# Kernel tuning notes

Measured on AMD Instinct MI355X. Metric: run time of the kernel, lower is better.

## Reference

```python
import jax, jax.numpy as jnp
import numpy as np

B, L, H, DI, N, R, K = 1, 1024, 2048, 4096, 16, 128, 4


def setup_inputs() -> dict:
    key = jax.random.key(0)
    ks = jax.random.split(key, 12)
    s = 0.02
    x = jax.random.normal(ks[0], (B, L, H), jnp.float32)
    W_in_states = jax.random.normal(ks[1], (DI, H), jnp.float32) * s
    W_in_gates = jax.random.normal(ks[2], (DI, H), jnp.float32) * s
    conv_w = jax.random.normal(ks[3], (DI, K), jnp.float32) * 0.2
    conv_b = jax.random.normal(ks[4], (DI,), jnp.float32) * 0.02
    W_dt = jax.random.normal(ks[5], (R, DI), jnp.float32) * s
    W_b = jax.random.normal(ks[6], (N, DI), jnp.float32) * s
    W_c = jax.random.normal(ks[7], (N, DI), jnp.float32) * s
    W_dtproj = jax.random.normal(ks[8], (DI, R), jnp.float32) * 0.1
    # dt bias so softplus(dt) is in a realistic small range
    b_dtproj = jax.random.uniform(ks[9], (DI,), jnp.float32, minval=-5.0, maxval=-3.0)
    A_log = jnp.log(jnp.broadcast_to(jnp.arange(1, N + 1, dtype=jnp.float32), (DI, N)))
    D = jnp.ones((DI,), jnp.float32)
    W_out = jax.random.normal(ks[10], (H, DI), jnp.float32) * s
    return {"x": x, "W_in_states": W_in_states, "W_in_gates": W_in_gates,
            "conv_w": conv_w, "conv_b": conv_b, "W_dt": W_dt, "W_b": W_b,
            "W_c": W_c, "W_dtproj": W_dtproj, "b_dtproj": b_dtproj,
            "A_log": A_log, "D": D, "W_out": W_out}


def _silu(v):
    return v * jax.nn.sigmoid(v)


def reference(x, W_in_states, W_in_gates, conv_w, conv_b, W_dt, W_b, W_c,
              W_dtproj, b_dtproj, A_log, D, W_out):
    b, l, _ = x.shape
    # input projections -> [B, DI, L]
    hs = jnp.einsum('blh,dh->bdl', x, W_in_states)
    gate = jnp.einsum('blh,dh->bdl', x, W_in_gates)
    # causal depthwise conv1d (kernel K, left pad K-1, truncate to L)
    k = conv_w.shape[-1]
    xpad = jnp.pad(hs, ((0, 0), (0, 0), (k - 1, 0)))
    conv = sum(conv_w[None, :, j, None] * xpad[:, :, j:j + l] for j in range(k))
    conv = conv + conv_b[None, :, None]
    hs = _silu(conv)                       # [B, DI, L]
    hst = hs.transpose(0, 2, 1)            # [B, L, DI]
    # data-dependent SSM params
    time_step = jnp.einsum('bld,rd->blr', hst, W_dt)           # [B, L, R]
    dt = jax.nn.softplus(time_step @ W_dtproj.T + b_dtproj)    # [B, L, DI]
    Bm = jnp.einsum('bld,nd->bln', hst, W_b)                   # [B, L, N]
    Cm = jnp.einsum('bld,nd->bln', hst, W_c)                   # [B, L, N]
    A = -jnp.exp(A_log)                                        # [DI, N]
    dt_bdl = dt.transpose(0, 2, 1)                             # [B, DI, L]
    dA = jnp.exp(A[None, :, None, :] * dt_bdl[:, :, :, None])  # [B, DI, L, N]
    dBu = dt_bdl[:, :, :, None] * Bm[:, None, :, :] * hs[:, :, :, None]
    # sequential selective scan over L
    dA_l = dA.transpose(2, 0, 1, 3)    # [L, B, DI, N]
    dBu_l = dBu.transpose(2, 0, 1, 3)

    def step(s, inp):
        a, bu = inp
        s = a * s + bu
        return s, s

    init = jnp.zeros((b, hs.shape[1], A_log.shape[1]), hs.dtype)
    _, h = jax.lax.scan(step, init, (dA_l, dBu_l))   # [L, B, DI, N]
    y = jnp.einsum('lbdn,bln->bdl', h, Cm)           # contract state dim
    y = y + hs * D[None, :, None]
    y = y * _silu(gate)
    out = jnp.einsum('bdl,od->blo', y, W_out)        # [B, L, H]
    return out
```

## Files before the change

### kernel.cpp

```cpp
#include <hip/hip_runtime.h>

#define SEQ 1024
#define HID 2048
#define DIN 4096
#define NST 16
#define RNK 128
#define CHN 32
#define CLEN 32

typedef __attribute__((ext_vector_type(4))) float f32x4;
typedef __attribute__((ext_vector_type(4))) __bf16 bf16x4v;
typedef __attribute__((ext_vector_type(8))) __bf16 bf16x8v;
typedef __attribute__((ext_vector_type(8))) unsigned short u16x8;

#define GPTR(p) ((const __attribute__((address_space(1))) void*)(p))
#define LPTR(p) ((__attribute__((address_space(3))) void*)(p))

__device__ __forceinline__ unsigned short f2bf(float v) {
  unsigned u = __builtin_bit_cast(unsigned, v);
  u = (u + 0x7fffu + ((u >> 16) & 1u)) >> 16;
  return (unsigned short)u;
}
__device__ __forceinline__ float softplus_f(float x) {
  return (x > 20.f) ? x : log1pf(__expf(x));
}
__device__ __forceinline__ float silu_f(float x) {
  return x / (1.f + __expf(-x));
}

#define CV_NX  (SEQ*HID)
#define CV_NW  (DIN*HID)
#define CV_NDT (RNK*DIN)
#define CV_NB  (NST*DIN)
#define CV_NPD (32*DIN)
#define CV_NWO (HID*DIN)
#define CV_TOT (CV_NX + 2*CV_NW + CV_NDT + 2*CV_NB + CV_NPD + CV_NDT + CV_NWO)

__global__ __launch_bounds__(256) void cvt_all(
    const float* __restrict__ x, const float* __restrict__ wis,
    const float* __restrict__ wig, const float* __restrict__ wdt,
    const float* __restrict__ wb, const float* __restrict__ wc,
    const float* __restrict__ wdtp, const float* __restrict__ wout,
    unsigned short* __restrict__ x_bf, unsigned short* __restrict__ wis_bf,
    unsigned short* __restrict__ wig_bf, unsigned short* __restrict__ wcat_bf,
    unsigned short* __restrict__ wdtp_bf, unsigned short* __restrict__ wout_bf)
{
  size_t j = ((size_t)blockIdx.x * 256 + threadIdx.x) * 16;
  const float* src = nullptr; unsigned short* dst;
  if (j < CV_NX) { src = x + j; dst = x_bf + j; }
  else if ((j -= CV_NX) < CV_NW) { src = wis + j; dst = wis_bf + j; }
  else if ((j -= CV_NW) < CV_NW) { src = wig + j; dst = wig_bf + j; }
  else if ((j -= CV_NW) < CV_NDT) { src = wdt + j; dst = wcat_bf + j; }
  else if ((j -= CV_NDT) < CV_NB) { src = wb + j; dst = wcat_bf + (size_t)128*DIN + j; }
  else if ((j -= CV_NB) < CV_NB) { src = wc + j; dst = wcat_bf + (size_t)144*DIN + j; }
  else if ((j -= CV_NB) < CV_NPD) { dst = wcat_bf + (size_t)160*DIN + j; }
  else if ((j -= CV_NPD) < CV_NDT) { src = wdtp + j; dst = wdtp_bf + j; }
  else { j -= CV_NDT; src = wout + j; dst = wout_bf + j; }
  u16x8 o0 = {}, o1 = {};
  if (src) {
    f32x4 a = *(const f32x4*)src;
    f32x4 b = *(const f32x4*)(src + 4);
    f32x4 c = *(const f32x4*)(src + 8);
    f32x4 d = *(const f32x4*)(src + 12);
#pragma unroll
    for (int i = 0; i < 4; i++) {
      o0[i] = f2bf(a[i]); o0[4 + i] = f2bf(b[i]);
      o1[i] = f2bf(c[i]); o1[4 + i] = f2bf(d[i]);
    }
  }
  *(u16x8*)dst = o0;
  *(u16x8*)(dst + 8) = o1;
}

template<int EPI>
__global__ __launch_bounds__(256) void gemm128(
    const unsigned short* __restrict__ Ag, const unsigned short* __restrict__ Bg,
    float* __restrict__ Cg, const float* __restrict__ bias,
    int Msz, int Nsz, int Kstride, int Kiter)
{
  __shared__ __align__(16) unsigned short As[2][128 * 64];
  __shared__ __align__(16) unsigned short Bs[2][128 * 64];
  const int kz = blockIdx.z;
  Ag += (size_t)kz * Kiter;
  Bg += (size_t)kz * Kiter;
  Cg += (size_t)kz * Msz * Nsz;
  const int nwg = gridDim.x * gridDim.y;
  const int orig = blockIdx.y * gridDim.x + blockIdx.x;
  const int swz = (orig & 7) * (nwg >> 3) + (orig >> 3);
  const int bx = swz % gridDim.x, by = swz / gridDim.x;
  const int tid = threadIdx.x;
  const int m0 = bx * 128, n0 = by * 128;
  const int lane = tid & 63, w = tid >> 6;
  const int wm = w >> 1, wn = w & 1;
  const int lg = lane >> 4, lr = lane & 15;
  const int srow = w * 32 + (lane >> 3);
  const int sslot = (lane & 7) ^ (lane >> 3);
  const unsigned short* Ag0 = Ag + (size_t)(m0 + srow) * Kstride + sslot * 8;
  const unsigned short* Bg0 = Bg + (size_t)(n0 + srow) * Kstride + sslot * 8;
  const int ldso = w * 2048;

  auto stage = [&](int b, int k0) {
#pragma unroll
    for (int i = 0; i < 4; i++)
      __builtin_amdgcn_global_load_lds(GPTR(Ag0 + (size_t)(i * 8) * Kstride + k0),
                                       LPTR(&As[b][ldso + i * 512]), 16, 0, 0);
#pragma unroll
    for (int i = 0; i < 4; i++)
      __builtin_amdgcn_global_load_lds(GPTR(Bg0 + (size_t)(i * 8) * Kstride + k0),
                                       LPTR(&Bs[b][ldso + i * 512]), 16, 0, 0);
  };

  const int nt = Kiter >> 6;
  stage(0, 0);
  f32x4 acc[4][4] = {};
  int cur = 0;
  const int rsw = lr & 7;
  for (int t = 0; t < nt; ++t) {
    asm volatile("s_waitcnt vmcnt(0)" ::: "memory");
    __builtin_amdgcn_s_barrier();
    asm volatile("" ::: "memory");
    if (t + 1 < nt) stage(cur ^ 1, (t + 1) * 64);
    bf16x8v af0[4], bf0[4], af1[4], bf1[4];
#pragma unroll
    for (int mi = 0; mi < 4; mi++) {
      const int row = (wm * 64 + mi * 16 + lr) * 64;
      af0[mi] = *(const bf16x8v*)&As[cur][row + ((0 * 4 + lg) ^ rsw) * 8];
      af1[mi] = *(const bf16x8v*)&As[cur][row + ((1 * 4 + lg) ^ rsw) * 8];
    }
#pragma unroll
    for (int ni = 0; ni < 4; ni++) {
      const int row = (wn * 64 + ni * 16 + lr) * 64;
      bf0[ni] = *(const bf16x8v*)&Bs[cur][row + ((0 * 4 + lg) ^ rsw) * 8];
      bf1[ni] = *(const bf16x8v*)&Bs[cur][row + ((1 * 4 + lg) ^ rsw) * 8];
    }
#pragma unroll
    for (int mi = 0; mi < 4; mi++)
#pragma unroll
      for (int ni = 0; ni < 4; ni++)
        acc[mi][ni] = __builtin_amdgcn_mfma_f32_16x16x32_bf16(af0[mi], bf0[ni], acc[mi][ni], 0, 0, 0);
#pragma unroll
    for (int mi = 0; mi < 4; mi++)
#pragma unroll
      for (int ni = 0; ni < 4; ni++)
        acc[mi][ni] = __builtin_amdgcn_mfma_f32_16x16x32_bf16(af1[mi], bf1[ni], acc[mi][ni], 0, 0, 0);
    cur ^= 1;
  }
#pragma unroll
  for (int mi = 0; mi < 4; mi++) {
#pragma unroll
    for (int ni = 0; ni < 4; ni++) {
      const int col = n0 + wn * 64 + ni * 16 + lr;
#pragma unroll
      for (int r = 0; r < 4; r++) {
        const int row = m0 + wm * 64 + mi * 16 + lg * 4 + r;
        float v = acc[mi][ni][r];
        if (EPI == 1) v = softplus_f(v + bias[col]);
        Cg[(size_t)row * Nsz + col] = v;
      }
    }
  }
}

template<int EPI>
__global__ __launch_bounds__(256) void gemm_nt(
    const unsigned short* __restrict__ Ag, const unsigned short* __restrict__ Bg,
    float* __restrict__ Cg, const float* __restrict__ bias,
    int Msz, int Nsz, int Kstride, int Kiter)
{
  __shared__ __align__(16) unsigned short As[128][40];
  __shared__ __align__(16) unsigned short Bs[64][40];
  const int kz = blockIdx.z;
  Ag += (size_t)kz * Kiter;
  Bg += (size_t)kz * Kiter;
  Cg += (size_t)kz * Msz * Nsz;
  const int tid = threadIdx.x;
  const int m0 = blockIdx.x * 128, n0 = blockIdx.y * 64;
  const int lane = tid & 63, w = tid >> 6;
  const int wm = w >> 1, wn = w & 1;
  const int lg = lane >> 4, lr = lane & 15;
  const int r4 = tid >> 2, c8 = (tid & 3) * 8;
  f32x4 acc[4][2] = {};
  for (int k0 = 0; k0 < Kiter; k0 += 32) {
    uint4 a0 = *(const uint4*)(Ag + (size_t)(m0 + r4) * Kstride + k0 + c8);
    uint4 a1 = *(const uint4*)(Ag + (size_t)(m0 + 64 + r4) * Kstride + k0 + c8);
    uint4 b0 = *(const uint4*)(Bg + (size_t)(n0 + r4) * Kstride + k0 + c8);
    *(uint4*)&As[r4][c8] = a0;
    *(uint4*)&As[64 + r4][c8] = a1;
    *(uint4*)&Bs[r4][c8] = b0;
    __syncthreads();
    bf16x8v af[4], bfr[2];
#pragma unroll
    for (int mi = 0; mi < 4; mi++) {
      const int row = wm * 64 + mi * 16 + lr;
      bf16x4v lo = *(const bf16x4v*)&As[row][4 * lg];
      bf16x4v hi = *(const bf16x4v*)&As[row][16 + 4 * lg];
      af[mi] = __builtin_shufflevector(lo, hi, 0, 1, 2, 3, 4, 5, 6, 7);
    }
#pragma unroll
    for (int ni = 0; ni < 2; ni++) {
      const int row = wn * 32 + ni * 16 + lr;
      bf16x4v lo = *(const bf16x4v*)&Bs[row][4 * lg];
      bf16x4v hi = *(const bf16x4v*)&Bs[row][16 + 4 * lg];
      bfr[ni] = __builtin_shufflevector(lo, hi, 0, 1, 2, 3, 4, 5, 6, 7);
    }
#pragma unroll
    for (int mi = 0; mi < 4; mi++)
#pragma unroll
      for (int ni = 0; ni < 2; ni++)
        acc[mi][ni] = __builtin_amdgcn_mfma_f32_16x16x32_bf16(af[mi], bfr[ni], acc[mi][ni], 0, 0, 0);
    __syncthreads();
  }
#pragma unroll
  for (int mi = 0; mi < 4; mi++) {
#pragma unroll
    for (int ni = 0; ni < 2; ni++) {
      const int col = n0 + wn * 32 + ni * 16 + lr;
#pragma unroll
      for (int r = 0; r < 4; r++) {
        const int row = m0 + wm * 64 + mi * 16 + lg * 4 + r;
        float v = acc[mi][ni][r];
        if (EPI == 1) v = softplus_f(v + bias[col]);
        Cg[(size_t)row * Nsz + col] = v;
      }
    }
  }
}

__global__ __launch_bounds__(256) void conv_silu(
    const float* __restrict__ pg, const float* __restrict__ cw,
    const float* __restrict__ cb, float* __restrict__ hs,
    unsigned short* __restrict__ hs_bf)
{
  int idx = blockIdx.x * 256 + threadIdx.x;
  int l = idx >> 12, d = idx & (DIN - 1);
  float acc = cb[d];
#pragma unroll
  for (int j = 0; j < 4; j++) {
    int ll = l + j - 3;
    float v = (ll >= 0) ? pg[(size_t)ll * 8192 + d] : 0.f;
    acc = fmaf(cw[d * 4 + j], v, acc);
  }
  float r = silu_f(acc);
  hs[idx] = r;
  hs_bf[idx] = f2bf(r);
}

__global__ __launch_bounds__(256) void reduce_ts(
    const float* __restrict__ c2p, float* __restrict__ c2,
    unsigned short* __restrict__ ts_bf)
{
  int i = blockIdx.x * 256 + threadIdx.x;
  float s = 0.f;
#pragma unroll
  for (int z = 0; z < 8; z++) s += c2p[(size_t)z * SEQ * 192 + i];
  c2[i] = s;
  int l = i / 192, col = i - l * 192;
  if (col < 128) ts_bf[l * 128 + col] = f2bf(s);
}

__global__ __launch_bounds__(256) void reduce_out(
    const float* __restrict__ p, float* __restrict__ out)
{
  int i = (blockIdx.x * 256 + threadIdx.x) * 4;
  float4 a = *(const float4*)&p[i];
#pragma unroll
  for (int z = 1; z < 4; z++) {
    float4 b = *(const float4*)&p[(size_t)z * SEQ * HID + i];
    a.x += b.x; a.y += b.y; a.z += b.z; a.w += b.w;
  }
  *(float4*)&out[i] = a;
}

__global__ __launch_bounds__(256) void scan_phase1(
    const float* __restrict__ dt, const float* __restrict__ hs,
    const float* __restrict__ c2, const float* __restrict__ alog,
    float* __restrict__ Pbuf, float* __restrict__ Sbuf)
{
  __shared__ float B_ch[CLEN][16];
  const int tid = threadIdx.x;
  const int d = blockIdx.x * 256 + tid;
  const int c = blockIdx.y;
  const int l0 = c * CLEN;
  for (int i = tid; i < CLEN * 16; i += 256)
    B_ch[i >> 4][i & 15] = c2[(size_t)(l0 + (i >> 4)) * 192 + 128 + (i & 15)];
  float a[16];
#pragma unroll
  for (int i = 0; i < 16; i++) a[i] = -__expf(alog[(size_t)d * 16 + i]);
  __syncthreads();
  float s[16] = {};
  float P[16];
#pragma unroll
  for (int i = 0; i < 16; i++) P[i] = 1.f;
  for (int t = 0; t < CLEN; t++) {
    float dtv = dt[(size_t)(l0 + t) * DIN + d];
    float u = hs[(size_t)(l0 + t) * DIN + d];
    float w = dtv * u;
#pragma unroll
    for (int n = 0; n < 16; n++) {
      float dA = __expf(a[n] * dtv);
      s[n] = fmaf(dA, s[n], w * B_ch[t][n]);
      P[n] *= dA;
    }
  }
  size_t base = ((size_t)c * DIN + d) * 16;
#pragma unroll
  for (int i = 0; i < 4; i++) {
    *(float4*)&Sbuf[base + 4 * i] = *(float4*)&s[4 * i];
    *(float4*)&Pbuf[base + 4 * i] = *(float4*)&P[4 * i];
  }
}

__global__ __launch_bounds__(256) void scan_phase2(
    const float* __restrict__ Pbuf, float* __restrict__ Sbuf)
{
  size_t idx = (size_t)blockIdx.x * 256 + threadIdx.x;
  const size_t stride = (size_t)DIN * 16;
  float s = 0.f;
#pragma unroll 4
  for (int c = 0; c < CHN; c++) {
    float Pv = Pbuf[c * stride + idx];
    float Sv = Sbuf[c * stride + idx];
    Sbuf[c * stride + idx] = s;
    s = fmaf(Pv, s, Sv);
  }
}

__global__ __launch_bounds__(256) void scan_phase3(
    const float* __restrict__ dt, const float* __restrict__ hs,
    const float* __restrict__ pg, const float* __restrict__ c2,
    const float* __restrict__ alog, const float* __restrict__ Dv,
    const float* __restrict__ sig, unsigned short* __restrict__ ygT)
{
  __shared__ float B_ch[CLEN][16], C_ch[CLEN][16];
  const int tid = threadIdx.x;
  const int d = blockIdx.x * 256 + tid;
  const int c = blockIdx.y;
  const int l0 = c * CLEN;
  for (int i = tid; i < CLEN * 16; i += 256) {
    int t = i >> 4, n = i & 15;
    B_ch[t][n] = c2[(size_t)(l0 + t) * 192 + 128 + n];
    C_ch[t][n] = c2[(size_t)(l0 + t) * 192 + 144 + n];
  }
  float a[16];
#pragma unroll
  for (int i = 0; i < 16; i++) a[i] = -__expf(alog[(size_t)d * 16 + i]);
  const float Dd = Dv[d];
  float s[16];
  size_t base = ((size_t)c * DIN + d) * 16;
#pragma unroll
  for (int i = 0; i < 4; i++) *(float4*)&s[4 * i] = *(const float4*)&sig[base + 4 * i];
  __syncthreads();
  for (int t = 0; t < CLEN; t++) {
    float dtv = dt[(size_t)(l0 + t) * DIN + d];
    float u = hs[(size_t)(l0 + t) * DIN + d];
    float g = pg[(size_t)(l0 + t) * 8192 + 4096 + d];
    float w = dtv * u;
    float y = 0.f;
#pragma unroll
    for (int n = 0; n < 16; n++) {
      float dA = __expf(a[n] * dtv);
      s[n] = fmaf(dA, s[n], w * B_ch[t][n]);
      y = fmaf(s[n], C_ch[t][n], y);
    }
    float o = (y + u * Dd) * silu_f(g);
    ygT[(size_t)(l0 + t) * DIN + d] = f2bf(o);
  }
}

extern "C" void kernel_launch(void* const* d_in, const int* in_sizes, int n_in,
                              void* d_out, int out_size, void* d_ws, size_t ws_size,
                              hipStream_t stream) {
  const float* x     = (const float*)d_in[0];
  const float* wis   = (const float*)d_in[1];
  const float* wig   = (const float*)d_in[2];
  const float* convw = (const float*)d_in[3];
  const float* convb = (const float*)d_in[4];
  const float* wdt   = (const float*)d_in[5];
  const float* wb    = (const float*)d_in[6];
  const float* wc    = (const float*)d_in[7];
  const float* wdtp  = (const float*)d_in[8];
  const float* bdtp  = (const float*)d_in[9];
  const float* alog  = (const float*)d_in[10];
  const float* Dv    = (const float*)d_in[11];
  const float* wout  = (const float*)d_in[12];

  char* ws = (char*)d_ws;
  size_t off = 0;
  auto alloc = [&](size_t bytes) { void* p = ws + off; off += (bytes + 255) & ~(size_t)255; return p; };
  unsigned short* x_bf    = (unsigned short*)alloc((size_t)SEQ * HID * 2);
  unsigned short* wis_bf  = (unsigned short*)alloc((size_t)DIN * HID * 2);
  unsigned short* wig_bf  = (unsigned short*)alloc((size_t)DIN * HID * 2);
  unsigned short* wcat_bf = (unsigned short*)alloc((size_t)192 * DIN * 2);
  unsigned short* wdtp_bf = (unsigned short*)alloc((size_t)DIN * RNK * 2);
  unsigned short* wout_bf = (unsigned short*)alloc((size_t)HID * DIN * 2);
  float* pg    = (float*)alloc((size_t)SEQ * 8192 * 4);
  float* hs2   = (float*)alloc((size_t)SEQ * DIN * 4);
  unsigned short* hs_bf = (unsigned short*)alloc((size_t)SEQ * DIN * 2);
  float* c2    = (float*)alloc((size_t)SEQ * 192 * 4);
  float* c2p   = (float*)alloc((size_t)8 * SEQ * 192 * 4);
  unsigned short* ts_bf = (unsigned short*)alloc((size_t)SEQ * RNK * 2);
  float* dtbuf = (float*)alloc((size_t)SEQ * DIN * 4);
  unsigned short* ygT_bf = (unsigned short*)alloc((size_t)SEQ * DIN * 2);
  if (off > ws_size) return;
  float* Pbuf = (float*)wis_bf;
  float* Sbuf = (float*)wig_bf;
  float* op_part = pg;

  cvt_all<<<CV_TOT / 4096, 256, 0, stream>>>(x, wis, wig, wdt, wb, wc, wdtp, wout,
                                             x_bf, wis_bf, wig_bf, wcat_bf, wdtp_bf, wout_bf);
  gemm128<0><<<dim3(SEQ / 128, 8192 / 128), 256, 0, stream>>>(x_bf, wis_bf, pg, nullptr, SEQ, 8192, HID, HID);
  conv_silu<<<(SEQ * DIN) / 256, 256, 0, stream>>>(pg, convw, convb, hs2, hs_bf);
  gemm_nt<0><<<dim3(SEQ / 128, 192 / 64, 8), 256, 0, stream>>>(hs_bf, wcat_bf, c2p, nullptr, SEQ, 192, DIN, DIN / 8);
  reduce_ts<<<(SEQ * 192) / 256, 256, 0, stream>>>(c2p, c2, ts_bf);
  gemm_nt<1><<<dim3(SEQ / 128, DIN / 64), 256, 0, stream>>>(ts_bf, wdtp_bf, dtbuf, bdtp, SEQ, DIN, RNK, RNK);
  scan_phase1<<<dim3(DIN / 256, CHN), 256, 0, stream>>>(dtbuf, hs2, c2, alog, Pbuf, Sbuf);
  scan_phase2<<<(DIN * NST) / 256, 256, 0, stream>>>(Pbuf, Sbuf);
  scan_phase3<<<dim3(DIN / 256, CHN), 256, 0, stream>>>(dtbuf, hs2, pg, c2, alog, Dv, Sbuf, ygT_bf);
  gemm128<0><<<dim3(SEQ / 128, HID / 128, 4), 256, 0, stream>>>(ygT_bf, wout_bf, op_part, nullptr, SEQ, HID, DIN, DIN / 4);
  reduce_out<<<(SEQ * HID) / 1024, 256, 0, stream>>>(op_part, (float*)d_out);
}
```

Measured before the change: 216.4 us.

## Widen gemm128 N-tile to 256 and make cvt_all grid-stride

The GEMM kernel's block tile grows from 128x128 to 128x256, so each wave computes 64x128 with 32 accumulators and reuses each A fragment across eight B fragments. This cuts LDS and global traffic per MFMA but raises register pressure and LDS use, and halves the block count for both large GEMMs. The fp32-to-bf16 conversion kernel becomes a grid-stride loop with a fixed 2048-block grid instead of one block per 4096 elements. The intent is to reduce launch and scheduling overhead there.

```diff
diff --git a/kernel.cpp b/kernel.cpp
--- a/kernel.cpp
+++ b/kernel.cpp
@@ -45,31 +45,34 @@
     unsigned short* __restrict__ wig_bf, unsigned short* __restrict__ wcat_bf,
     unsigned short* __restrict__ wdtp_bf, unsigned short* __restrict__ wout_bf)
 {
-  size_t j = ((size_t)blockIdx.x * 256 + threadIdx.x) * 16;
-  const float* src = nullptr; unsigned short* dst;
-  if (j < CV_NX) { src = x + j; dst = x_bf + j; }
-  else if ((j -= CV_NX) < CV_NW) { src = wis + j; dst = wis_bf + j; }
-  else if ((j -= CV_NW) < CV_NW) { src = wig + j; dst = wig_bf + j; }
-  else if ((j -= CV_NW) < CV_NDT) { src = wdt + j; dst = wcat_bf + j; }
-  else if ((j -= CV_NDT) < CV_NB) { src = wb + j; dst = wcat_bf + (size_t)128*DIN + j; }
-  else if ((j -= CV_NB) < CV_NB) { src = wc + j; dst = wcat_bf + (size_t)144*DIN + j; }
-  else if ((j -= CV_NB) < CV_NPD) { dst = wcat_bf + (size_t)160*DIN + j; }
-  else if ((j -= CV_NPD) < CV_NDT) { src = wdtp + j; dst = wdtp_bf + j; }
-  else { j -= CV_NDT; src = wout + j; dst = wout_bf + j; }
-  u16x8 o0 = {}, o1 = {};
-  if (src) {
-    f32x4 a = *(const f32x4*)src;
-    f32x4 b = *(const f32x4*)(src + 4);
-    f32x4 c = *(const f32x4*)(src + 8);
-    f32x4 d = *(const f32x4*)(src + 12);
-#pragma unroll
-    for (int i = 0; i < 4; i++) {
-      o0[i] = f2bf(a[i]); o0[4 + i] = f2bf(b[i]);
-      o1[i] = f2bf(c[i]); o1[4 + i] = f2bf(d[i]);
-    }
-  }
-  *(u16x8*)dst = o0;
-  *(u16x8*)(dst + 8) = o1;
+  const size_t stride = (size_t)gridDim.x * 256 * 16;
+  for (size_t j0 = ((size_t)blockIdx.x * 256 + threadIdx.x) * 16; j0 < CV_TOT; j0 += stride) {
+    size_t j = j0;
+    const float* src = nullptr; unsigned short* dst;
+    if (j < CV_NX) { src = x + j; dst = x_bf + j; }
+    else if ((j -= CV_NX) < CV_NW) { src = wis + j; dst = wis_bf + j; }
+    else if ((j -= CV_NW) < CV_NW) { src = wig + j; dst = wig_bf + j; }
+    else if ((j -= CV_NW) < CV_NDT) { src = wdt + j; dst = wcat_bf + j; }
+    else if ((j -= CV_NDT) < CV_NB) { src = wb + j; dst = wcat_bf + (size_t)128*DIN + j; }
+    else if ((j -= CV_NB) < CV_NB) { src = wc + j; dst = wcat_bf + (size_t)144*DIN + j; }
+    else if ((j -= CV_NB) < CV_NPD) { dst = wcat_bf + (size_t)160*DIN + j; }
+    else if ((j -= CV_NPD) < CV_NDT) { src = wdtp + j; dst = wdtp_bf + j; }
+    else { j -= CV_NDT; src = wout + j; dst = wout_bf + j; }
+    u16x8 o0 = {}, o1 = {};
+    if (src) {
+      f32x4 a = *(const f32x4*)src;
+      f32x4 b = *(const f32x4*)(src + 4);
+      f32x4 c = *(const f32x4*)(src + 8);
+      f32x4 d = *(const f32x4*)(src + 12);
+#pragma unroll
+      for (int i = 0; i < 4; i++) {
+        o0[i] = f2bf(a[i]); o0[4 + i] = f2bf(b[i]);
+        o1[i] = f2bf(c[i]); o1[4 + i] = f2bf(d[i]);
+      }
+    }
+    *(u16x8*)dst = o0;
+    *(u16x8*)(dst + 8) = o1;
+  }
 }
 
 template<int EPI>
@@ -79,7 +82,7 @@
     int Msz, int Nsz, int Kstride, int Kiter)
 {
   __shared__ __align__(16) unsigned short As[2][128 * 64];
-  __shared__ __align__(16) unsigned short Bs[2][128 * 64];
+  __shared__ __align__(16) unsigned short Bs[2][256 * 64];
   const int kz = blockIdx.z;
   Ag += (size_t)kz * Kiter;
   Bg += (size_t)kz * Kiter;
@@ -89,30 +92,32 @@
   const int swz = (orig & 7) * (nwg >> 3) + (orig >> 3);
   const int bx = swz % gridDim.x, by = swz / gridDim.x;
   const int tid = threadIdx.x;
-  const int m0 = bx * 128, n0 = by * 128;
+  const int m0 = bx * 128, n0 = by * 256;
   const int lane = tid & 63, w = tid >> 6;
   const int wm = w >> 1, wn = w & 1;
   const int lg = lane >> 4, lr = lane & 15;
-  const int srow = w * 32 + (lane >> 3);
+  const int sA = w * 32 + (lane >> 3);
+  const int sB = w * 64 + (lane >> 3);
   const int sslot = (lane & 7) ^ (lane >> 3);
-  const unsigned short* Ag0 = Ag + (size_t)(m0 + srow) * Kstride + sslot * 8;
-  const unsigned short* Bg0 = Bg + (size_t)(n0 + srow) * Kstride + sslot * 8;
-  const int ldso = w * 2048;
+  const unsigned short* Ag0 = Ag + (size_t)(m0 + sA) * Kstride + sslot * 8;
+  const unsigned short* Bg0 = Bg + (size_t)(n0 + sB) * Kstride + sslot * 8;
+  const int ldA = w * 2048;
+  const int ldB = w * 4096;
 
   auto stage = [&](int b, int k0) {
 #pragma unroll
     for (int i = 0; i < 4; i++)
       __builtin_amdgcn_global_load_lds(GPTR(Ag0 + (size_t)(i * 8) * Kstride + k0),
-                                       LPTR(&As[b][ldso + i * 512]), 16, 0, 0);
-#pragma unroll
-    for (int i = 0; i < 4; i++)
+                                       LPTR(&As[b][ldA + i * 512]), 16, 0, 0);
+#pragma unroll
+    for (int i = 0; i < 8; i++)
       __builtin_amdgcn_global_load_lds(GPTR(Bg0 + (size_t)(i * 8) * Kstride + k0),
-                                       LPTR(&Bs[b][ldso + i * 512]), 16, 0, 0);
+                                       LPTR(&Bs[b][ldB + i * 512]), 16, 0, 0);
   };
 
   const int nt = Kiter >> 6;
   stage(0, 0);
-  f32x4 acc[4][4] = {};
+  f32x4 acc[4][8] = {};
   int cur = 0;
   const int rsw = lr & 7;
   for (int t = 0; t < nt; ++t) {
@@ -120,36 +125,28 @@
     __builtin_amdgcn_s_barrier();
     asm volatile("" ::: "memory");
     if (t + 1 < nt) stage(cur ^ 1, (t + 1) * 64);
-    bf16x8v af0[4], bf0[4], af1[4], bf1[4];
-#pragma unroll
-    for (int mi = 0; mi < 4; mi++) {
-      const int row = (wm * 64 + mi * 16 + lr) * 64;
-      af0[mi] = *(const bf16x8v*)&As[cur][row + ((0 * 4 + lg) ^ rsw) * 8];
-      af1[mi] = *(const bf16x8v*)&As[cur][row + ((1 * 4 + lg) ^ rsw) * 8];
-    }
-#pragma unroll
-    for (int ni = 0; ni < 4; ni++) {
-      const int row = (wn * 64 + ni * 16 + lr) * 64;
-      bf0[ni] = *(const bf16x8v*)&Bs[cur][row + ((0 * 4 + lg) ^ rsw) * 8];
-      bf1[ni] = *(const bf16x8v*)&Bs[cur][row + ((1 * 4 + lg) ^ rsw) * 8];
-    }
-#pragma unroll
-    for (int mi = 0; mi < 4; mi++)
-#pragma unroll
-      for (int ni = 0; ni < 4; ni++)
-        acc[mi][ni] = __builtin_amdgcn_mfma_f32_16x16x32_bf16(af0[mi], bf0[ni], acc[mi][ni], 0, 0, 0);
-#pragma unroll
-    for (int mi = 0; mi < 4; mi++)
-#pragma unroll
-      for (int ni = 0; ni < 4; ni++)
-        acc[mi][ni] = __builtin_amdgcn_mfma_f32_16x16x32_bf16(af1[mi], bf1[ni], acc[mi][ni], 0, 0, 0);
+#pragma unroll
+    for (int kk = 0; kk < 2; kk++) {
+      bf16x8v af[4], bf[8];
+#pragma unroll
+      for (int mi = 0; mi < 4; mi++)
+        af[mi] = *(const bf16x8v*)&As[cur][(wm * 64 + mi * 16 + lr) * 64 + ((kk * 4 + lg) ^ rsw) * 8];
+#pragma unroll
+      for (int ni = 0; ni < 8; ni++)
+        bf[ni] = *(const bf16x8v*)&Bs[cur][(wn * 128 + ni * 16 + lr) * 64 + ((kk * 4 + lg) ^ rsw) * 8];
+#pragma unroll
+      for (int mi = 0; mi < 4; mi++)
+#pragma unroll
+        for (int ni = 0; ni < 8; ni++)
+          acc[mi][ni] = __builtin_amdgcn_mfma_f32_16x16x32_bf16(af[mi], bf[ni], acc[mi][ni], 0, 0, 0);
+    }
     cur ^= 1;
   }
 #pragma unroll
   for (int mi = 0; mi < 4; mi++) {
 #pragma unroll
-    for (int ni = 0; ni < 4; ni++) {
-      const int col = n0 + wn * 64 + ni * 16 + lr;
+    for (int ni = 0; ni < 8; ni++) {
+      const int col = n0 + wn * 128 + ni * 16 + lr;
 #pragma unroll
       for (int r = 0; r < 4; r++) {
         const int row = m0 + wm * 64 + mi * 16 + lg * 4 + r;
@@ -406,9 +403,9 @@
   float* Sbuf = (float*)wig_bf;
   float* op_part = pg;
 
-  cvt_all<<<CV_TOT / 4096, 256, 0, stream>>>(x, wis, wig, wdt, wb, wc, wdtp, wout,
-                                             x_bf, wis_bf, wig_bf, wcat_bf, wdtp_bf, wout_bf);
-  gemm128<0><<<dim3(SEQ / 128, 8192 / 128), 256, 0, stream>>>(x_bf, wis_bf, pg, nullptr, SEQ, 8192, HID, HID);
+  cvt_all<<<2048, 256, 0, stream>>>(x, wis, wig, wdt, wb, wc, wdtp, wout,
+                                    x_bf, wis_bf, wig_bf, wcat_bf, wdtp_bf, wout_bf);
+  gemm128<0><<<dim3(SEQ / 128, 8192 / 256), 256, 0, stream>>>(x_bf, wis_bf, pg, nullptr, SEQ, 8192, HID, HID);
   conv_silu<<<(SEQ * DIN) / 256, 256, 0, stream>>>(pg, convw, convb, hs2, hs_bf);
   gemm_nt<0><<<dim3(SEQ / 128, 192 / 64, 8), 256, 0, stream>>>(hs_bf, wcat_bf, c2p, nullptr, SEQ, 192, DIN, DIN / 8);
   reduce_ts<<<(SEQ * 192) / 256, 256, 0, stream>>>(c2p, c2, ts_bf);
@@ -416,6 +413,6 @@
   scan_phase1<<<dim3(DIN / 256, CHN), 256, 0, stream>>>(dtbuf, hs2, c2, alog, Pbuf, Sbuf);
   scan_phase2<<<(DIN * NST) / 256, 256, 0, stream>>>(Pbuf, Sbuf);
   scan_phase3<<<dim3(DIN / 256, CHN), 256, 0, stream>>>(dtbuf, hs2, pg, c2, alog, Dv, Sbuf, ygT_bf);
-  gemm128<0><<<dim3(SEQ / 128, HID / 128, 4), 256, 0, stream>>>(ygT_bf, wout_bf, op_part, nullptr, SEQ, HID, DIN, DIN / 4);
+  gemm128<0><<<dim3(SEQ / 128, HID / 256, 4), 256, 0, stream>>>(ygT_bf, wout_bf, op_part, nullptr, SEQ, HID, DIN, DIN / 4);
   reduce_out<<<(SEQ * HID) / 1024, 256, 0, stream>>>(op_part, (float*)d_out);
 }
```

Measured after the change: 237.9 us. +9.9%, slower.

## Enlarge GEMM tiles to 256x256 with 512 threads and add split-K

Applied to the files above, without the earlier changes.

Replaces the 128x128 bf16 MFMA GEMM with a 256x256 tile run by 512 threads (8 waves, each computing 128x64). The input projection now uses split-K=2, and the output projection moves from split-K=4 to 8, so each launch has 256 workgroups. The conv and scan kernels add the two input-projection partials on read, and the final reduction sums 8 partials. Larger tiles cut global/LDS reloads per FLOP, but they use 128KB of LDS per block, limiting occupancy to one block per CU. Extra fp32 partial traffic and a doubled workspace are also added.

```diff
diff --git a/kernel.cpp b/kernel.cpp
--- a/kernel.cpp
+++ b/kernel.cpp
@@ -73,13 +73,13 @@
 }
 
 template<int EPI>
-__global__ __launch_bounds__(256) void gemm128(
+__global__ __launch_bounds__(512, 2) void gemm256(
     const unsigned short* __restrict__ Ag, const unsigned short* __restrict__ Bg,
     float* __restrict__ Cg, const float* __restrict__ bias,
     int Msz, int Nsz, int Kstride, int Kiter)
 {
-  __shared__ __align__(16) unsigned short As[2][128 * 64];
-  __shared__ __align__(16) unsigned short Bs[2][128 * 64];
+  __shared__ __align__(16) unsigned short As[2][256 * 64];
+  __shared__ __align__(16) unsigned short Bs[2][256 * 64];
   const int kz = blockIdx.z;
   Ag += (size_t)kz * Kiter;
   Bg += (size_t)kz * Kiter;
@@ -89,9 +89,9 @@
   const int swz = (orig & 7) * (nwg >> 3) + (orig >> 3);
   const int bx = swz % gridDim.x, by = swz / gridDim.x;
   const int tid = threadIdx.x;
-  const int m0 = bx * 128, n0 = by * 128;
+  const int m0 = bx * 256, n0 = by * 256;
   const int lane = tid & 63, w = tid >> 6;
-  const int wm = w >> 1, wn = w & 1;
+  const int wm = w >> 2, wn = w & 3;
   const int lg = lane >> 4, lr = lane & 15;
   const int srow = w * 32 + (lane >> 3);
   const int sslot = (lane & 7) ^ (lane >> 3);
@@ -112,7 +112,7 @@
 
   const int nt = Kiter >> 6;
   stage(0, 0);
-  f32x4 acc[4][4] = {};
+  f32x4 acc[8][4] = {};
   int cur = 0;
   const int rsw = lr & 7;
   for (int t = 0; t < nt; ++t) {
@@ -120,39 +120,31 @@
     __builtin_amdgcn_s_barrier();
     asm volatile("" ::: "memory");
     if (t + 1 < nt) stage(cur ^ 1, (t + 1) * 64);
-    bf16x8v af0[4], bf0[4], af1[4], bf1[4];
-#pragma unroll
-    for (int mi = 0; mi < 4; mi++) {
-      const int row = (wm * 64 + mi * 16 + lr) * 64;
-      af0[mi] = *(const bf16x8v*)&As[cur][row + ((0 * 4 + lg) ^ rsw) * 8];
-      af1[mi] = *(const bf16x8v*)&As[cur][row + ((1 * 4 + lg) ^ rsw) * 8];
-    }
-#pragma unroll
-    for (int ni = 0; ni < 4; ni++) {
-      const int row = (wn * 64 + ni * 16 + lr) * 64;
-      bf0[ni] = *(const bf16x8v*)&Bs[cur][row + ((0 * 4 + lg) ^ rsw) * 8];
-      bf1[ni] = *(const bf16x8v*)&Bs[cur][row + ((1 * 4 + lg) ^ rsw) * 8];
-    }
-#pragma unroll
-    for (int mi = 0; mi < 4; mi++)
+#pragma unroll
+    for (int kk = 0; kk < 2; kk++) {
+      bf16x8v af[8], bf[4];
+#pragma unroll
+      for (int mi = 0; mi < 8; mi++)
+        af[mi] = *(const bf16x8v*)&As[cur][(wm * 128 + mi * 16 + lr) * 64 + ((kk * 4 + lg) ^ rsw) * 8];
 #pragma unroll
       for (int ni = 0; ni < 4; ni++)
-        acc[mi][ni] = __builtin_amdgcn_mfma_f32_16x16x32_bf16(af0[mi], bf0[ni], acc[mi][ni], 0, 0, 0);
-#pragma unroll
-    for (int mi = 0; mi < 4; mi++)
-#pragma unroll
-      for (int ni = 0; ni < 4; ni++)
-        acc[mi][ni] = __builtin_amdgcn_mfma_f32_16x16x32_bf16(af1[mi], bf1[ni], acc[mi][ni], 0, 0, 0);
+        bf[ni] = *(const bf16x8v*)&Bs[cur][(wn * 64 + ni * 16 + lr) * 64 + ((kk * 4 + lg) ^ rsw) * 8];
+#pragma unroll
+      for (int mi = 0; mi < 8; mi++)
+#pragma unroll
+        for (int ni = 0; ni < 4; ni++)
+          acc[mi][ni] = __builtin_amdgcn_mfma_f32_16x16x32_bf16(af[mi], bf[ni], acc[mi][ni], 0, 0, 0);
+    }
     cur ^= 1;
   }
 #pragma unroll
-  for (int mi = 0; mi < 4; mi++) {
+  for (int mi = 0; mi < 8; mi++) {
 #pragma unroll
     for (int ni = 0; ni < 4; ni++) {
       const int col = n0 + wn * 64 + ni * 16 + lr;
 #pragma unroll
       for (int r = 0; r < 4; r++) {
-        const int row = m0 + wm * 64 + mi * 16 + lg * 4 + r;
+        const int row = m0 + wm * 128 + mi * 16 + lg * 4 + r;
         float v = acc[mi][ni][r];
         if (EPI == 1) v = softplus_f(v + bias[col]);
         Cg[(size_t)row * Nsz + col] = v;
@@ -231,13 +223,14 @@
     const float* __restrict__ cb, float* __restrict__ hs,
     unsigned short* __restrict__ hs_bf)
 {
+  const size_t ZOFF = (size_t)SEQ * 8192;
   int idx = blockIdx.x * 256 + threadIdx.x;
   int l = idx >> 12, d = idx & (DIN - 1);
   float acc = cb[d];
 #pragma unroll
   for (int j = 0; j < 4; j++) {
     int ll = l + j - 3;
-    float v = (ll >= 0) ? pg[(size_t)ll * 8192 + d] : 0.f;
+    float v = (ll >= 0) ? pg[(size_t)ll * 8192 + d] + pg[ZOFF + (size_t)ll * 8192 + d] : 0.f;
     acc = fmaf(cw[d * 4 + j], v, acc);
   }
   float r = silu_f(acc);
@@ -264,7 +257,7 @@
   int i = (blockIdx.x * 256 + threadIdx.x) * 4;
   float4 a = *(const float4*)&p[i];
 #pragma unroll
-  for (int z = 1; z < 4; z++) {
+  for (int z = 1; z < 8; z++) {
     float4 b = *(const float4*)&p[(size_t)z * SEQ * HID + i];
     a.x += b.x; a.y += b.y; a.z += b.z; a.w += b.w;
   }
@@ -332,6 +325,7 @@
     const float* __restrict__ sig, unsigned short* __restrict__ ygT)
 {
   __shared__ float B_ch[CLEN][16], C_ch[CLEN][16];
+  const size_t ZOFF = (size_t)SEQ * 8192;
   const int tid = threadIdx.x;
   const int d = blockIdx.x * 256 + tid;
   const int c = blockIdx.y;
@@ -353,7 +347,8 @@
   for (int t = 0; t < CLEN; t++) {
     float dtv = dt[(size_t)(l0 + t) * DIN + d];
     float u = hs[(size_t)(l0 + t) * DIN + d];
-    float g = pg[(size_t)(l0 + t) * 8192 + 4096 + d];
+    size_t goff = (size_t)(l0 + t) * 8192 + 4096 + d;
+    float g = pg[goff] + pg[ZOFF + goff];
     float w = dtv * u;
     float y = 0.f;
 #pragma unroll
@@ -393,7 +388,7 @@
   unsigned short* wcat_bf = (unsigned short*)alloc((size_t)192 * DIN * 2);
   unsigned short* wdtp_bf = (unsigned short*)alloc((size_t)DIN * RNK * 2);
   unsigned short* wout_bf = (unsigned short*)alloc((size_t)HID * DIN * 2);
-  float* pg    = (float*)alloc((size_t)SEQ * 8192 * 4);
+  float* pg    = (float*)alloc((size_t)2 * SEQ * 8192 * 4);
   float* hs2   = (float*)alloc((size_t)SEQ * DIN * 4);
   unsigned short* hs_bf = (unsigned short*)alloc((size_t)SEQ * DIN * 2);
   float* c2    = (float*)alloc((size_t)SEQ * 192 * 4);
@@ -408,7 +403,7 @@
 
   cvt_all<<<CV_TOT / 4096, 256, 0, stream>>>(x, wis, wig, wdt, wb, wc, wdtp, wout,
                                              x_bf, wis_bf, wig_bf, wcat_bf, wdtp_bf, wout_bf);
-  gemm128<0><<<dim3(SEQ / 128, 8192 / 128), 256, 0, stream>>>(x_bf, wis_bf, pg, nullptr, SEQ, 8192, HID, HID);
+  gemm256<0><<<dim3(SEQ / 256, 8192 / 256, 2), 512, 0, stream>>>(x_bf, wis_bf, pg, nullptr, SEQ, 8192, HID, HID / 2);
   conv_silu<<<(SEQ * DIN) / 256, 256, 0, stream>>>(pg, convw, convb, hs2, hs_bf);
   gemm_nt<0><<<dim3(SEQ / 128, 192 / 64, 8), 256, 0, stream>>>(hs_bf, wcat_bf, c2p, nullptr, SEQ, 192, DIN, DIN / 8);
   reduce_ts<<<(SEQ * 192) / 256, 256, 0, stream>>>(c2p, c2, ts_bf);
@@ -416,6 +411,6 @@
   scan_phase1<<<dim3(DIN / 256, CHN), 256, 0, stream>>>(dtbuf, hs2, c2, alog, Pbuf, Sbuf);
   scan_phase2<<<(DIN * NST) / 256, 256, 0, stream>>>(Pbuf, Sbuf);
   scan_phase3<<<dim3(DIN / 256, CHN), 256, 0, stream>>>(dtbuf, hs2, pg, c2, alog, Dv, Sbuf, ygT_bf);
-  gemm128<0><<<dim3(SEQ / 128, HID / 128, 4), 256, 0, stream>>>(ygT_bf, wout_bf, op_part, nullptr, SEQ, HID, DIN, DIN / 4);
+  gemm256<0><<<dim3(SEQ / 256, HID / 256, 8), 512, 0, stream>>>(ygT_bf, wout_bf, op_part, nullptr, SEQ, HID, DIN, DIN / 8);
   reduce_out<<<(SEQ * HID) / 1024, 256, 0, stream>>>(op_part, (float*)d_out);
 }
```

After: 235.4 us. +8.8%, slower.
